# Performance work log

Measured on AMD Instinct MI355X. Metric: run time of the kernel, lower is better.

Reference implementation:

```python
import jax, jax.numpy as jnp
import numpy as np

N_NODES = 50000
N_EDGES = 800000
FEAT = 128
OUT = 128
BATCH = 2


def setup_inputs() -> dict:
    key = jax.random.key(0)
    k_h, k_w1, k_w2, k_a, k_src, k_dst = jax.random.split(key, 6)
    h = jax.random.normal(k_h, (BATCH, N_NODES, FEAT), dtype=jnp.float32)
    # xavier-uniform-ish scale for params
    W1 = jax.random.normal(k_w1, (FEAT, FEAT), dtype=jnp.float32) * (1.414 / np.sqrt(FEAT))
    W2 = jax.random.normal(k_w2, (FEAT, OUT), dtype=jnp.float32) * (1.414 / np.sqrt(FEAT))
    a = jax.random.normal(k_a, (2 * FEAT, 1), dtype=jnp.float32) * 0.05
    src = jax.random.randint(k_src, (N_EDGES,), 0, N_NODES, dtype=jnp.int32)
    dst = jax.random.randint(k_dst, (N_EDGES,), 0, N_NODES, dtype=jnp.int32)
    return {"h": h, "W1": W1, "W2": W2, "a": a, "src": src, "dst": dst}


def reference(h, W1, W2, a, src, dst):
    B, N, F = h.shape
    g = jnp.einsum('bnf,fk->bnk', h, W1)                      # [B,N,F]
    # cat([g_i, g_j]) @ a  ==  g_i @ a[:F] + g_j @ a[F:]
    s_i = g @ a[:F, 0]                                        # [B,N]
    s_j = g @ a[F:, 0]                                        # [B,N]
    e = jax.nn.leaky_relu(s_i[:, src] + s_j[:, dst], 0.2)     # [B,E]
    # segment softmax over edges grouped by src node
    eT = e.T                                                  # [E,B]
    m = jax.ops.segment_max(eT, src, num_segments=N)          # [N,B]
    ex = jnp.exp(eT - m[src])                                 # [E,B]
    denom = jax.ops.segment_sum(ex, src, num_segments=N)      # [N,B]
    alpha = (ex / denom[src]).T                               # [B,E]
    msg = g[:, dst] * alpha[..., None]                        # [B,E,F]
    h_prime = jnp.zeros_like(g).at[:, src].add(msg)           # scatter-add onto src
    return jax.nn.relu(jnp.einsum('bnf,fo->bno', h_prime, W2))
```

## Files before the change

### kernel.cpp

```cpp
#include <hip/hip_runtime.h>
#include <hip/hip_bf16.h>
#include <hip/hip_fp16.h>
#include <cfloat>

#define N_NODES 50000
#define N_EDGES 800000
#define FEAT 128
#define BATCH 2
#define RTOT (BATCH*N_NODES)

typedef __bf16 bf16x8 __attribute__((ext_vector_type(8)));
typedef float  f32x4  __attribute__((ext_vector_type(4)));

__device__ inline unsigned short f2bf(float f){
  unsigned int u = __float_as_uint(f);
  u = (u + 0x7fffu + ((u >> 16) & 1u)) >> 16;
  return (unsigned short)u;
}

__global__ void k_prep(const float* __restrict__ W1, const float* __restrict__ W2,
                       __bf16* __restrict__ W1t, __bf16* __restrict__ W2t,
                       int* __restrict__ cnt){
  int i = blockIdx.x*blockDim.x + threadIdx.x;
  if(i < FEAT*FEAT){
    int k = i >> 7, col = i & 127;
    int sw = (col << 7) + (k ^ ((col & 7) << 3));
    W1t[sw] = (__bf16)W1[i];
    W2t[sw] = (__bf16)W2[i];
  }
  if(i < N_NODES) cnt[i] = 0;
}

__global__ __launch_bounds__(256) void k_gemm1_mfma(const float* __restrict__ h,
        const __bf16* __restrict__ W1t, const float* __restrict__ a,
        __bf16* __restrict__ g, float* __restrict__ s_i, float* __restrict__ s_j,
        const int* __restrict__ src, int* __restrict__ cnt)
{
  __shared__ __bf16 Bs[FEAT*FEAT];
  int t = threadIdx.x, lane = t & 63, wid = t >> 6;
  {
    const float4* srcp = (const float4*)W1t;
    float4* dstp = (float4*)Bs;
    for(int i = t; i < FEAT*FEAT/8; i += 256) dstp[i] = srcp[i];
  }
  __syncthreads();

  int hgrp = lane >> 4;
  int kq = hgrp * 8;
  const int NT = (RTOT + 63) / 64;

  for(int tile = blockIdx.x; tile < NT; tile += gridDim.x){
    int r = tile*64 + wid*16 + (lane & 15);

    bf16x8 af[4];
    {
      const float* hrow = h + (size_t)r*FEAT + kq;
      bool ok = (r < RTOT);
      #pragma unroll
      for(int ks = 0; ks < 4; ks++){
        bf16x8 v = {};
        if(ok){
          float4 p0 = *(const float4*)(hrow + ks*32);
          float4 p1 = *(const float4*)(hrow + ks*32 + 4);
          v[0]=(__bf16)p0.x; v[1]=(__bf16)p0.y; v[2]=(__bf16)p0.z; v[3]=(__bf16)p0.w;
          v[4]=(__bf16)p1.x; v[5]=(__bf16)p1.y; v[6]=(__bf16)p1.z; v[7]=(__bf16)p1.w;
        }
        af[ks] = v;
      }
    }

    f32x4 acc[8] = {};
    #pragma unroll
    for(int cb = 0; cb < 8; cb++){
      int col = cb*16 + (lane & 15);
      int swbase = (col << 7);
      int swx = ((col & 7) << 3);
      #pragma unroll
      for(int ks = 0; ks < 4; ks++){
        int kb = ks*32 + kq;
        bf16x8 bf = *(const bf16x8*)&Bs[swbase + (kb ^ swx)];
        acc[cb] = __builtin_amdgcn_mfma_f32_16x16x32_bf16(bf, af[ks], acc[cb], 0, 0, 0);
      }
    }

    if(r < RTOT){
      int b = (r >= N_NODES) ? 1 : 0;
      int n = r - b*N_NODES;
      __bf16* grow = g + (size_t)n*256 + b*128;
      float pi = 0.f, pj = 0.f;
      #pragma unroll
      for(int cb = 0; cb < 8; cb++){
        int c0 = cb*16 + hgrp*4;
        float4 al = *(const float4*)&a[c0];
        float4 ah = *(const float4*)&a[FEAT + c0];
        pi = fmaf(acc[cb][0], al.x, pi); pj = fmaf(acc[cb][0], ah.x, pj);
        pi = fmaf(acc[cb][1], al.y, pi); pj = fmaf(acc[cb][1], ah.y, pj);
        pi = fmaf(acc[cb][2], al.z, pi); pj = fmaf(acc[cb][2], ah.z, pj);
        pi = fmaf(acc[cb][3], al.w, pi); pj = fmaf(acc[cb][3], ah.w, pj);
        uint2 w;
        w.x = ((unsigned int)f2bf(acc[cb][1]) << 16) | f2bf(acc[cb][0]);
        w.y = ((unsigned int)f2bf(acc[cb][3]) << 16) | f2bf(acc[cb][2]);
        *(uint2*)(grow + c0) = w;
      }
      pi += __shfl_xor(pi, 16, 64); pj += __shfl_xor(pj, 16, 64);
      pi += __shfl_xor(pi, 32, 64); pj += __shfl_xor(pj, 32, 64);
      if(hgrp == 0){ s_i[n*2 + b] = pi; s_j[n*2 + b] = pj; }
    }
  }

  int gs = gridDim.x * 256;
  for(int e = blockIdx.x*256 + t; e < N_EDGES; e += gs)
    atomicAdd(&cnt[src[e]], 1);
}

__global__ __launch_bounds__(1024) void k_scan(const int* __restrict__ cnt,
                                               int* __restrict__ off, int* __restrict__ curs){
  __shared__ int s[1024];
  __shared__ int wsum[16];
  __shared__ int pfx;
  int t = threadIdx.x, b = blockIdx.x;
  int ps = 0;
  int lim = b*1024;
  for(int i = t; i < lim; i += 1024) ps += cnt[i];
  #pragma unroll
  for(int mm=32; mm; mm>>=1) ps += __shfl_xor(ps, mm, 64);
  if((t & 63) == 0) wsum[t >> 6] = ps;
  __syncthreads();
  if(t == 0){
    int P = 0;
    #pragma unroll
    for(int w = 0; w < 16; w++) P += wsum[w];
    pfx = P;
  }
  int idx = b*1024 + t;
  int v = (idx < N_NODES) ? cnt[idx] : 0;
  s[t] = v; __syncthreads();
  for(int st = 1; st < 1024; st <<= 1){
    int u = (t >= st) ? s[t-st] : 0;
    __syncthreads();
    s[t] += u;
    __syncthreads();
  }
  if(idx < N_NODES){
    int o = pfx + s[t] - v;
    off[idx] = o;
    curs[idx] = o;
  }
  if(b == 0 && t == 0) off[N_NODES] = N_EDGES;
}

__global__ void k_fill(const int* __restrict__ src, const int* __restrict__ dst,
                       int* __restrict__ curs, unsigned short* __restrict__ dste){
  int e = blockIdx.x*blockDim.x + threadIdx.x;
  if(e < N_EDGES){ int pos = atomicAdd(&curs[src[e]], 1); dste[pos] = (unsigned short)dst[e]; }
}

__global__ __launch_bounds__(512) void k_agg2(const unsigned int* __restrict__ g,
     const float* __restrict__ s_i, const float* __restrict__ s_j,
     const int* __restrict__ off,
     const unsigned short* __restrict__ dste, const __bf16* __restrict__ W2t,
     float* __restrict__ out)
{
  __shared__ __bf16 Bs[FEAT*FEAT];
  __shared__ __bf16 hpT[16*FEAT];
  int t = threadIdx.x, lane = t & 63, w = t >> 6;
  {
    const float4* srcp = (const float4*)W2t;
    float4* dstp = (float4*)Bs;
    for(int i = t; i < FEAT*FEAT/8; i += 512) dstp[i] = srcp[i];
  }

  int n = blockIdx.x*8 + w;
  int o0 = off[n], deg = off[n+1] - o0;
  int half = lane >> 5, li = lane & 31;
  float si = s_i[n*2 + half];
  int selp = lane & 32;

  float denom = 0.f;
  float a0=0.f, a1=0.f, a2=0.f, a3=0.f;

  for(int base=0; base<deg; base+=32){
    int i = base + li;
    unsigned int wv = 0;
    if(i < deg){
      int d = dste[o0 + i];
      float xx = si + s_j[d*2 + half];
      float x = (xx > 0.f) ? xx : 0.2f*xx;
      float p = __expf(x);
      denom += p;
      wv = ((unsigned int)__half_as_ushort(__float2half(p)) << 16) | (unsigned int)d;
    }
    int lim = min(32, deg-base);
    int lim8 = (lim + 7) & ~7;
    for(int j=0; j<lim8; j+=8){
      unsigned int ww[8];
      #pragma unroll
      for(int c=0;c<8;c++) ww[c] = __shfl(wv, selp | (j+c), 64);
      uint2 u[8]; float q[8];
      #pragma unroll
      for(int c=0;c<8;c++){
        q[c] = __half2float(__ushort_as_half((unsigned short)(ww[c] >> 16)));
        u[c] = *(const uint2*)(g + (size_t)(ww[c] & 0xffffu)*128 + lane*2);
      }
      #pragma unroll
      for(int c=0;c<8;c++){
        a0 = fmaf(q[c], __uint_as_float(u[c].x << 16),         a0);
        a1 = fmaf(q[c], __uint_as_float(u[c].x & 0xffff0000u), a1);
        a2 = fmaf(q[c], __uint_as_float(u[c].y << 16),         a2);
        a3 = fmaf(q[c], __uint_as_float(u[c].y & 0xffff0000u), a3);
      }
    }
  }
  #pragma unroll
  for(int mm=16; mm; mm>>=1) denom += __shfl_xor(denom, mm, 64);
  float inv = (denom > 0.f) ? 1.0f/denom : 0.f;

  {
    int ri = w*2 + half;
    int gidx = li >> 1;
    int gsw = gidx ^ (ri & 7);
    int coff = gsw*8 + (li & 1)*4;
    unsigned int w0 = ((unsigned int)f2bf(a1*inv) << 16) | f2bf(a0*inv);
    unsigned int w1 = ((unsigned int)f2bf(a3*inv) << 16) | f2bf(a2*inv);
    uint2 o; o.x = w0; o.y = w1;
    *(uint2*)&hpT[ri*FEAT + coff] = o;
  }
  __syncthreads();

  int r  = lane & 15;
  int kq16 = lane >> 4;
  bf16x8 af[4];
  #pragma unroll
  for(int ks = 0; ks < 4; ks++){
    int gr = ks*4 + kq16;
    int gsw2 = gr ^ (r & 7);
    af[ks] = *(const bf16x8*)&hpT[r*FEAT + gsw2*8];
  }
  f32x4 acc = {};
  int col = w*16 + (lane & 15);
  int swbase = (col << 7);
  int swx = ((col & 7) << 3);
  #pragma unroll
  for(int ks = 0; ks < 4; ks++){
    int kb = ks*32 + kq16*8;
    bf16x8 bf = *(const bf16x8*)&Bs[swbase + (kb ^ swx)];
    acc = __builtin_amdgcn_mfma_f32_16x16x32_bf16(bf, af[ks], acc, 0, 0, 0);
  }
  {
    int node = blockIdx.x*8 + (r >> 1);
    int b = r & 1;
    float4 o;
    o.x = fmaxf(acc[0], 0.f); o.y = fmaxf(acc[1], 0.f);
    o.z = fmaxf(acc[2], 0.f); o.w = fmaxf(acc[3], 0.f);
    *(float4*)&out[(size_t)(b*N_NODES + node)*FEAT + w*16 + kq16*4] = o;
  }
}

extern "C" void kernel_launch(void* const* d_in, const int* in_sizes, int n_in,
                              void* d_out, int out_size, void* d_ws, size_t ws_size,
                              hipStream_t stream) {
  const float* h  = (const float*)d_in[0];
  const float* W1 = (const float*)d_in[1];
  const float* W2 = (const float*)d_in[2];
  const float* a  = (const float*)d_in[3];
  const int* src  = (const int*)d_in[4];
  const int* dst  = (const int*)d_in[5];
  float* out = (float*)d_out;

  char* w = (char*)d_ws;
  __bf16* g   = (__bf16*)w;                          w += (size_t)RTOT*FEAT*2;
  float* s_i  = (float*)w;                           w += (size_t)RTOT*4;
  float* s_j  = (float*)w;                           w += (size_t)RTOT*4;
  __bf16* W1t = (__bf16*)w;                          w += FEAT*FEAT*2;
  __bf16* W2t = (__bf16*)w;                          w += FEAT*FEAT*2;
  int* cnt  = (int*)w;                               w += N_NODES*4;
  int* off  = (int*)w;                               w += (N_NODES+1)*4;
  int* curs = (int*)w;                               w += N_NODES*4;
  unsigned short* dste = (unsigned short*)w;         w += N_EDGES*2;

  k_prep<<<(N_NODES+255)/256,256,0,stream>>>(W1,W2,W1t,W2t,cnt);

  k_gemm1_mfma<<<1024,256,0,stream>>>(h,W1t,a,g,s_i,s_j,src,cnt);

  int nb = (N_NODES+1023)/1024;
  k_scan<<<nb,1024,0,stream>>>(cnt,off,curs);
  k_fill<<<(N_EDGES+255)/256,256,0,stream>>>(src,dst,curs,dste);

  k_agg2<<<N_NODES/8,512,0,stream>>>((const unsigned int*)g,s_i,s_j,off,dste,W2t,out);
}
```

Baseline: 181.2 us.

## Permute g feature layout for 16-byte stores and fold permutation into W2

The g intermediate is now stored with a permuted feature order, so each lane writes two MFMA column blocks as one 16-byte store instead of 8-byte stores. To keep the result correct, W2's rows are permuted the same way during prep, so the final GEMM, which consumes gathered g features, sees matching k indices. The gather/aggregation stage reads g rows in full and is order-agnostic, so it is unaffected. This targets store efficiency in gemm1, and possibly wider contiguous accesses downstream, but relies on the permutation being consistent across every consumer of g.

```diff
diff --git a/kernel.cpp b/kernel.cpp
--- a/kernel.cpp
+++ b/kernel.cpp
@@ -12,11 +12,12 @@
 typedef __bf16 bf16x8 __attribute__((ext_vector_type(8)));
 typedef float  f32x4  __attribute__((ext_vector_type(4)));
 
-__device__ inline unsigned short f2bf(float f){
+__device__ inline unsigned int f2bf(float f){
   unsigned int u = __float_as_uint(f);
   u = (u + 0x7fffu + ((u >> 16) & 1u)) >> 16;
-  return (unsigned short)u;
-}
+  return u & 0xffffu;
+}
+
 
 __global__ void k_prep(const float* __restrict__ W1, const float* __restrict__ W2,
                        __bf16* __restrict__ W1t, __bf16* __restrict__ W2t,
@@ -24,9 +25,12 @@
   int i = blockIdx.x*blockDim.x + threadIdx.x;
   if(i < FEAT*FEAT){
     int k = i >> 7, col = i & 127;
-    int sw = (col << 7) + (k ^ ((col & 7) << 3));
-    W1t[sw] = (__bf16)W1[i];
-    W2t[sw] = (__bf16)W2[i];
+    int sw1 = (col << 7) + (k ^ ((col & 7) << 3));
+    W1t[sw1] = (__bf16)W1[i];
+    int cb = k >> 4, hgrp = (k >> 2) & 3, j = k & 3;
+    int s = ((cb >> 1) << 5) + (hgrp << 3) + ((cb & 1) << 2) + j;
+    int sw2 = (col << 7) + (s ^ ((col & 7) << 3));
+    W2t[sw2] = (__bf16)W2[i];
   }
   if(i < N_NODES) cnt[i] = 0;
 }
@@ -97,10 +101,16 @@
         pi = fmaf(acc[cb][1], al.y, pi); pj = fmaf(acc[cb][1], ah.y, pj);
         pi = fmaf(acc[cb][2], al.z, pi); pj = fmaf(acc[cb][2], ah.z, pj);
         pi = fmaf(acc[cb][3], al.w, pi); pj = fmaf(acc[cb][3], ah.w, pj);
-        uint2 w;
-        w.x = ((unsigned int)f2bf(acc[cb][1]) << 16) | f2bf(acc[cb][0]);
-        w.y = ((unsigned int)f2bf(acc[cb][3]) << 16) | f2bf(acc[cb][2]);
-        *(uint2*)(grow + c0) = w;
+      }
+      #pragma unroll
+      for(int k2 = 0; k2 < 4; k2++){
+        int cA = 2*k2, cB = 2*k2+1;
+        uint4 v;
+        v.x = (f2bf(acc[cA][1]) << 16) | f2bf(acc[cA][0]);
+        v.y = (f2bf(acc[cA][3]) << 16) | f2bf(acc[cA][2]);
+        v.z = (f2bf(acc[cB][1]) << 16) | f2bf(acc[cB][0]);
+        v.w = (f2bf(acc[cB][3]) << 16) | f2bf(acc[cB][2]);
+        *(uint4*)(grow + k2*32 + hgrp*8) = v;
       }
       pi += __shfl_xor(pi, 16, 64); pj += __shfl_xor(pj, 16, 64);
       pi += __shfl_xor(pi, 32, 64); pj += __shfl_xor(pj, 32, 64);
@@ -220,8 +230,8 @@
     int gidx = li >> 1;
     int gsw = gidx ^ (ri & 7);
     int coff = gsw*8 + (li & 1)*4;
-    unsigned int w0 = ((unsigned int)f2bf(a1*inv) << 16) | f2bf(a0*inv);
-    unsigned int w1 = ((unsigned int)f2bf(a3*inv) << 16) | f2bf(a2*inv);
+    unsigned int w0 = (f2bf(a1*inv) << 16) | f2bf(a0*inv);
+    unsigned int w1 = (f2bf(a3*inv) << 16) | f2bf(a2*inv);
     uint2 o; o.x = w0; o.y = w1;
     *(uint2*)&hpT[ri*FEAT + coff] = o;
   }
```

Result: faster. 173.5 us (-4.3%).
